# Performance work log

Hardware: AMD Instinct MI355X
Metric: run time of the kernel (lower is better)

Reference implementation:

```python
import jax, jax.numpy as jnp
import numpy as np

NEG_INF = -1e30
NEG_SLOPE = 0.2


def setup_inputs() -> dict:
    key = jax.random.key(0)
    k1, k2, k3, k4, k5 = jax.random.split(key, 5)
    B, N, D, H = 2, 2048, 512, 8
    k = D // H
    return {
        "x": jax.random.normal(k1, (B, N, D), dtype=jnp.float32),
        "A": jax.random.randint(k2, (B, N, N), 0, 2, dtype=jnp.int32),
        "W_proj": jax.random.normal(k3, (D, D), dtype=jnp.float32) * (1.0 / np.sqrt(D)),
        "W_att": jax.random.normal(k4, (H, 2 * k), dtype=jnp.float32) * (1.0 / np.sqrt(2 * k)),
        "b_att": jax.random.normal(k5, (H,), dtype=jnp.float32) * 0.01,
    }


def reference(x, A, W_proj, W_att, b_att):
    # x: [B, N, D_in]; A: [B, N, N]; W_proj: [D_in, D_out]; W_att: [H, 2k]; b_att: [H]
    B, N, _ = x.shape
    H, two_k = W_att.shape
    k = two_k // 2
    xp = jnp.einsum('bnd,do->bno', x, W_proj)            # [B, N, H*k]
    xh = xp.reshape(B, N, H, k).transpose(0, 2, 1, 3)    # [B, H, N, k]
    # Additive attention: score(i,j) = leaky_relu(w[:k]@x_i + w[k:]@x_j + b).
    # Decompose instead of materializing the O(N^2 * 2k) concat tensor.
    a_src = jnp.einsum('bhnk,hk->bhn', xh, W_att[:, :k])  # contribution of node i
    a_dst = jnp.einsum('bhnk,hk->bhn', xh, W_att[:, k:])  # contribution of node j
    scores = a_src[:, :, :, None] + a_dst[:, :, None, :] + b_att[None, :, None, None]
    scores = jax.nn.leaky_relu(scores, negative_slope=NEG_SLOPE)  # [B, H, N, N]
    mask = (A > 0)[:, None, :, :]
    scores = jnp.where(mask, scores, NEG_INF)
    att = jax.nn.softmax(scores, axis=-1)
    out = jax.nn.relu(jnp.einsum('bhij,bhjk->bhik', att, xh))  # [B, H, N, k]
    return out.transpose(0, 2, 1, 3).reshape(B, N, H * k)
```

## Files before the change

kernel.cpp:

```cpp
#include <hip/hip_runtime.h>
#include <cstdint>
#include <cstddef>

#define NEG_SLOPE 0.2f
#define LOG2E 1.4426950408889634f

#define BB 2
#define NN 2048
#define DD 512
#define HH 8
#define KK 64

typedef _Float16 half8 __attribute__((ext_vector_type(8)));
typedef _Float16 half4 __attribute__((ext_vector_type(4)));
typedef _Float16 half2v __attribute__((ext_vector_type(2)));
typedef float floatx4 __attribute__((ext_vector_type(4)));

#define X16T_OFF  ((size_t)0)
#define WT_OFF    ((size_t)4194304)
#define XHT_OFF   ((size_t)4718592)
#define ASRC_OFF  ((size_t)8912896)
#define AFP_OFF   ((size_t)9043968)
#define AFM_OFF   ((size_t)9109504)
#define ADMAX_OFF ((size_t)9175040)
#define MW_OFF    ((size_t)9183232)

#if __has_builtin(__builtin_amdgcn_global_load_lds)
#define GLL(gsrc, lbase, lane) \
    __builtin_amdgcn_global_load_lds((const __attribute__((address_space(1))) void*)(gsrc), \
                                     (__attribute__((address_space(3))) void*)(lbase), 16, 0, 0)
#else
#define GLL(gsrc, lbase, lane) \
    (*(uint4*)((char*)(lbase) + (size_t)(lane) * 16) = *(const uint4*)(gsrc))
#endif

__device__ __forceinline__ unsigned pkmm(unsigned Ep2, unsigned fp,
                                         unsigned Em2, unsigned fm) {
    union U { unsigned u; half2v h; };
    U a, b, c, d, r;
    a.u = Ep2; b.u = fp; c.u = Em2; d.u = fm;
    r.h = __builtin_elementwise_max(a.h * b.h, c.h * d.h);
    return r.u;
}

__global__ __launch_bounds__(256) void k_prep(const float* __restrict__ x,
                                              const float* __restrict__ Wp,
                                              _Float16* __restrict__ x16t,
                                              _Float16* __restrict__ WT) {
    __shared__ float tile[64][65];
    const int tid = threadIdx.x;
    const int bi = blockIdx.x;
    if (bi < 256) {
        const int r = tid & 15, cg = tid >> 4;
        const float* srow = x + (size_t)(bi * 16 + r) * DD;
        _Float16* obase = x16t + ((size_t)bi * 64) * 128 + r * 8;
#pragma unroll
        for (int q = 0; q < 4; ++q) {
            const int chunk = q * 16 + cg;
            float4 v0 = *(const float4*)(srow + chunk * 8);
            float4 v1 = *(const float4*)(srow + chunk * 8 + 4);
            half8 hv;
            hv[0] = (_Float16)v0.x; hv[1] = (_Float16)v0.y;
            hv[2] = (_Float16)v0.z; hv[3] = (_Float16)v0.w;
            hv[4] = (_Float16)v1.x; hv[5] = (_Float16)v1.y;
            hv[6] = (_Float16)v1.z; hv[7] = (_Float16)v1.w;
            *(half8*)(obase + (size_t)chunk * 128) = hv;
        }
    } else {
        const int wb = bi - 256;
        const int d0 = (wb >> 3) * 64, o0 = (wb & 7) * 64;
        const int r = tid >> 2, cq = tid & 3;
#pragma unroll
        for (int qq = 0; qq < 4; ++qq) {
            float4 v = *(const float4*)&Wp[(size_t)(d0 + r) * DD + o0 + cq * 16 + qq * 4];
            tile[r][cq * 16 + qq * 4 + 0] = v.x;
            tile[r][cq * 16 + qq * 4 + 1] = v.y;
            tile[r][cq * 16 + qq * 4 + 2] = v.z;
            tile[r][cq * 16 + qq * 4 + 3] = v.w;
        }
        __syncthreads();
#pragma unroll
        for (int qq = 0; qq < 2; ++qq) {
            half8 hv;
#pragma unroll
            for (int e = 0; e < 8; ++e) hv[e] = (_Float16)tile[cq * 16 + qq * 8 + e][r];
            *(half8*)&WT[(size_t)(o0 + r) * DD + d0 + cq * 16 + qq * 8] = hv;
        }
    }
}

__global__ __launch_bounds__(256) void k_pj(const int* __restrict__ A,
                                            const _Float16* __restrict__ x16t,
                                            const _Float16* __restrict__ WT,
                                            const float* __restrict__ Watt,
                                            unsigned long long* __restrict__ mwT,
                                            _Float16* __restrict__ xhT2,
                                            float* __restrict__ asrc,
                                            unsigned* __restrict__ aFp_g,
                                            unsigned* __restrict__ aFm_g,
                                            float* __restrict__ admax) {
    __shared__ __align__(16) char smem[65536];
    const int tid = threadIdx.x;
    const int bi = blockIdx.x;
    const int r3 = bi % 3;

    if (r3 != 2) {
        unsigned long long (*mwt)[4] = (unsigned long long (*)[4])smem;
        const int mid = (bi / 3) * 2 + r3;
        const int w = tid >> 6, lane = tid & 63;
        const int b = mid >> 9, n0 = (mid & 511) * 4;
        const int* Arow = A + ((size_t)b * NN + n0 + w) * NN + lane;
        int v[32];
#pragma unroll
        for (int c = 0; c < 32; ++c) v[c] = Arow[c * 64];
#pragma unroll
        for (int c = 0; c < 32; ++c) {
            unsigned long long m = __ballot(v[c] != 0);
            if (lane == 0) mwt[c][w] = m;
        }
        __syncthreads();
        if (tid < 128) {
            const int c = tid >> 2, rl = tid & 3;
            mwT[((size_t)b * 32 + c) * NN + n0 + rl] = mwt[c][rl];
        }
        return;
    }

    _Float16* bt = (_Float16*)smem;
    const int pid = bi / 3;
    const int mtile = pid >> 3, h = pid & 7;
    const int m0 = mtile * 64;
    {
        const int cir = tid & 63, wv4 = tid >> 6;
        const char* gsrc = (const char*)(WT + (size_t)h * 64 * DD);
        char* lbase = (char*)bt;
#pragma unroll
        for (int q = 0; q < 16; ++q) {
            const int row = q * 4 + wv4;
            *(uint4*)(lbase + row * 1024 + ((cir ^ (row & 7)) * 16)) =
                *(const uint4*)(gsrc + (size_t)row * 1024 + cir * 16);
        }
    }
    __syncthreads();
    const int w = tid >> 6, l = tid & 63, li = l & 15, p = l >> 4;
    const char* bbase = (const char*)bt;
    const _Float16* abase = x16t + ((size_t)(mtile * 4 + w)) * 64 * 128 + li * 8;
    floatx4 acc[4] = {};
    for (int k0 = 0; k0 < DD; k0 += 32) {
        const int ch = (k0 >> 3) + p;
        half8 a = *(const half8*)(abase + (size_t)ch * 128);
#pragma unroll
        for (int ct = 0; ct < 4; ++ct) {
            const int row = ct * 16 + li;
            half8 bfr = *(const half8*)(bbase + row * 1024 + ((ch ^ (li & 7)) * 16));
            acc[ct] = __builtin_amdgcn_mfma_f32_16x16x32_f16(a, bfr, acc[ct], 0, 0, 0);
        }
    }
    const int b = m0 >> 11, n0m = m0 & (NN - 1);
    const int c = n0m >> 6;
    const int bh = b * HH + h;
    {
        char* tb2 = (char*)xhT2 + ((size_t)(bh * 32 + c)) * 8192;
        const int colchunk = w * 2 + (p >> 1);
        const int sub = (p & 1) * 8;
#pragma unroll
        for (int ct = 0; ct < 4; ++ct) {
            const int kk = ct * 16 + li;
            half4 hv;
#pragma unroll
            for (int r = 0; r < 4; ++r) hv[r] = (_Float16)acc[ct][r];
            *(half4*)(tb2 + kk * 128 + ((colchunk ^ (kk & 7)) << 4) + sub) = hv;
        }
    }
    float w1[4], w2[4];
#pragma unroll
    for (int ct = 0; ct < 4; ++ct) {
        w1[ct] = Watt[h * 128 + ct * 16 + li];
        w2[ct] = Watt[h * 128 + 64 + ct * 16 + li];
    }
    float s1v[4], s2v[4];
    float mx = -1e30f;
#pragma unroll
    for (int r = 0; r < 4; ++r) {
        float s1 = 0.f, s2 = 0.f;
#pragma unroll
        for (int ct = 0; ct < 4; ++ct) { s1 += acc[ct][r] * w1[ct]; s2 += acc[ct][r] * w2[ct]; }
#pragma unroll
        for (int d = 1; d < 16; d <<= 1) { s1 += __shfl_xor(s1, d, 64); s2 += __shfl_xor(s2, d, 64); }
        s1v[r] = s1; s2v[r] = s2;
        mx = fmaxf(mx, s2);
    }
    mx = fmaxf(mx, __shfl_xor(mx, 16, 64));
    mx = fmaxf(mx, __shfl_xor(mx, 32, 64));
    if (l == 0) admax[bh * 128 + (mtile & 31) * 4 + w] = mx;
    if (li == 0) {
        const int nb = n0m + w * 16 + p * 4;
        *(float4*)&asrc[bh * NN + nb] = make_float4(s1v[0], s1v[1], s1v[2], s1v[3]);
        union { half2v h; unsigned u; } q;
        unsigned fpw[2], fmw[2];
#pragma unroll
        for (int pr = 0; pr < 2; ++pr) {
            q.h[0] = (_Float16)exp2f(s2v[2 * pr] * LOG2E);
            q.h[1] = (_Float16)exp2f(s2v[2 * pr + 1] * LOG2E);
            fpw[pr] = q.u;
            q.h[0] = (_Float16)exp2f(NEG_SLOPE * s2v[2 * pr] * LOG2E);
            q.h[1] = (_Float16)exp2f(NEG_SLOPE * s2v[2 * pr + 1] * LOG2E);
            fmw[pr] = q.u;
        }
        const int wb = (bh * NN + nb) >> 1;
        *(uint2*)&aFp_g[wb] = make_uint2(fpw[0], fpw[1]);
        *(uint2*)&aFm_g[wb] = make_uint2(fmw[0], fmw[1]);
    }
}

__global__ __launch_bounds__(256) void k_attn(const _Float16* __restrict__ xhT2,
                                              const float* __restrict__ asrc,
                                              const unsigned* __restrict__ aFp,
                                              const unsigned* __restrict__ aFm,
                                              const float* __restrict__ admax,
                                              const unsigned long long* __restrict__ mwT,
                                              const float* __restrict__ batt,
                                              float* __restrict__ out) {
    __shared__ __align__(16) _Float16 vt[2][2][4096];
    __shared__ __align__(16) unsigned aFpl[2][2][32];
    __shared__ __align__(16) unsigned aFml[2][2][32];
    __shared__ unsigned long long mwl[2][2][32];
    __shared__ float accd_s[2][16];
    __shared__ float amx_s;

    const int tid = threadIdx.x;
    const int w = tid >> 6, l = tid & 63, li = l & 15, p = l >> 4;
    const int g = w & 1, wr = w >> 1;
    const int bid = blockIdx.x;
    const int bh = bid >> 6, it = bid & 63;
    const int b = bh >> 3, h = bh & (HH - 1);
    const int i0 = it * 32;

    const _Float16* vbase = xhT2 + (size_t)bh * 32 * 4096;

    {
#pragma unroll
        for (int q = 0; q < 4; ++q) {
            const int chunk = (wr * 4 + q) * 64 + l;
            GLL(vbase + (size_t)g * 4096 + chunk * 8, &vt[g][0][(wr * 4 + q) * 512], l);
        }
        if (tid < 128) {
            const int arr = tid >> 6, par = (tid >> 5) & 1, wd = tid & 31;
            const unsigned v = (arr ? aFm : aFp)[bh * 1024 + par * 32 + wd];
            if (arr) aFml[par][0][wd] = v; else aFpl[par][0][wd] = v;
        }
        if (tid < 64) mwl[tid >> 5][0][tid & 31] =
            mwT[((size_t)b * 32 + (tid >> 5)) * NN + i0 + (tid & 31)];
    }
    if (w == 0) {
        float mx = fmaxf(admax[bh * 128 + l], admax[bh * 128 + 64 + l]);
#pragma unroll
        for (int d = 1; d < 64; d <<= 1) mx = fmaxf(mx, __shfl_xor(mx, d, 64));
        if (l == 0) amx_s = mx;
    }
    __syncthreads();

    const float am = amx_s;
    const float bbv = batt[h];
    const int i = i0 + wr * 16 + li;
    const float ai = (asrc[bh * NN + i] + bbv) * LOG2E;
    const float tb = ai + am * LOG2E;
    const float Mi = fmaxf(tb, NEG_SLOPE * tb);
    union { half2v h; unsigned u; } epk, emk;
    epk.h[0] = epk.h[1] = (_Float16)exp2f(ai - Mi);
    emk.h[0] = emk.h[1] = (_Float16)exp2f(NEG_SLOPE * ai - Mi);
    const unsigned Ep2 = epk.u, Em2 = emk.u;
    floatx4 acc[4] = {};
    floatx4 accd = {};
    half8 ones;
#pragma unroll
    for (int e = 0; e < 8; ++e) ones[e] = (_Float16)1.0f;

    unsigned raf = 0; unsigned long long rmw = 0;
    for (int ci = 0; ci < 16; ++ci) {
        const int buf = ci & 1;
        char* vtg = (char*)&vt[g][buf][0];
        if (ci < 15) {
            const int cb = 2 * (ci + 1);
            const int cn = cb + g;
#pragma unroll
            for (int q = 0; q < 4; ++q) {
                const int chunk = (wr * 4 + q) * 64 + l;
                GLL(vbase + (size_t)cn * 4096 + chunk * 8, &vt[g][buf ^ 1][(wr * 4 + q) * 512], l);
            }
            if (tid < 128) {
                const int arr = tid >> 6, par = (tid >> 5) & 1, wd = tid & 31;
                raf = (arr ? aFm : aFp)[bh * 1024 + (cb + par) * 32 + wd];
            }
            if (tid < 64) rmw = mwT[((size_t)b * 32 + cb + (tid >> 5)) * NN + i0 + (tid & 31)];
        }
        const unsigned long long mword = mwl[g][buf][wr * 16 + li];
#pragma unroll
        for (int js = 0; js < 2; ++js) {
            const int wb = js * 16 + p * 4;
            const uint4 Fp4 = *(const uint4*)&aFpl[g][buf][wb];
            const uint4 Fm4 = *(const uint4*)&aFml[g][buf][wb];
            const unsigned m8 = (unsigned)(mword >> (js * 32 + p * 8)) & 0xFFu;
            const unsigned fpv[4] = {Fp4.x, Fp4.y, Fp4.z, Fp4.w};
            const unsigned fmv[4] = {Fm4.x, Fm4.y, Fm4.z, Fm4.w};
            union { unsigned u[4]; half8 h; } afu;
#pragma unroll
            for (int pi = 0; pi < 4; ++pi) {
                const unsigned m2 = (m8 >> (2 * pi)) & 3u;
                const unsigned mk = ((m2 & 1u) ? 0x0000FFFFu : 0u) |
                                    ((m2 & 2u) ? 0xFFFF0000u : 0u);
                afu.u[pi] = pkmm(Ep2, fpv[pi], Em2, fmv[pi]) & mk;
            }
            const half8 af = afu.h;
            accd = __builtin_amdgcn_mfma_f32_16x16x32_f16(af, ones, accd, 0, 0, 0);
#pragma unroll
            for (int ct = 0; ct < 4; ++ct) {
                const half8 bf = *(const half8*)(vtg + (ct * 16 + li) * 128 +
                                                 (((js * 4 + p) ^ (li & 7)) << 4));
                acc[ct] = __builtin_amdgcn_mfma_f32_16x16x32_f16(af, bf, acc[ct], 0, 0, 0);
            }
        }
        if (ci < 15) {
            if (tid < 128) {
                const int arr = tid >> 6, par = (tid >> 5) & 1, wd = tid & 31;
                if (arr) aFml[par][buf ^ 1][wd] = raf; else aFpl[par][buf ^ 1][wd] = raf;
            }
            if (tid < 64) mwl[tid >> 5][buf ^ 1][tid & 31] = rmw;
        }
        __syncthreads();
    }

    float* accs = (float*)&vt[0][0][0];
    if (g == 1) {
#pragma unroll
        for (int ct = 0; ct < 4; ++ct)
#pragma unroll
            for (int r = 0; r < 4; ++r)
                accs[(wr * 16 + p * 4 + r) * 64 + ct * 16 + li] = acc[ct][r];
        if (li == 0) {
#pragma unroll
            for (int r = 0; r < 4; ++r) accd_s[wr][p * 4 + r] = accd[r];
        }
    }
    __syncthreads();
    if (g == 0) {
#pragma unroll
        for (int r = 0; r < 4; ++r) {
            const float d = accd[r] + accd_s[wr][p * 4 + r];
            const float inv = 1.f / fmaxf(d, 1e-30f);
            const int irow = i0 + wr * 16 + p * 4 + r;
            float* orow = out + ((size_t)b * NN + irow) * DD + h * KK;
#pragma unroll
            for (int ct = 0; ct < 4; ++ct) {
                const float v = (acc[ct][r] + accs[(wr * 16 + p * 4 + r) * 64 + ct * 16 + li]) * inv;
                orow[ct * 16 + li] = fmaxf(v, 0.f);
            }
        }
    }
}

extern "C" void kernel_launch(void* const* d_in, const int* in_sizes, int n_in,
                              void* d_out, int out_size, void* d_ws, size_t ws_size,
                              hipStream_t stream) {
    const float* x    = (const float*)d_in[0];
    const int*   A    = (const int*)d_in[1];
    const float* Wp   = (const float*)d_in[2];
    const float* Watt = (const float*)d_in[3];
    const float* batt = (const float*)d_in[4];
    float* out = (float*)d_out;

    char* ws = (char*)d_ws;
    _Float16* x16t = (_Float16*)(ws + X16T_OFF);
    _Float16* WT   = (_Float16*)(ws + WT_OFF);
    _Float16* xhT2 = (_Float16*)(ws + XHT_OFF);
    float* asrc  = (float*)(ws + ASRC_OFF);
    unsigned* aFp = (unsigned*)(ws + AFP_OFF);
    unsigned* aFm = (unsigned*)(ws + AFM_OFF);
    float* admax = (float*)(ws + ADMAX_OFF);
    unsigned long long* mwT = (unsigned long long*)(ws + MW_OFF);

    k_prep<<<dim3(320), 256, 0, stream>>>(x, Wp, x16t, WT);
    k_pj<<<dim3(1536), 256, 0, stream>>>(A, x16t, WT, Watt, mwT, xhT2, asrc, aFp, aFm, admax);
    k_attn<<<dim3(BB * HH * 64), 256, 0, stream>>>(xhT2, asrc, aFp, aFm, admax, mwT, batt, out);
}
```

Baseline: 51.67 us.

## Triple-buffer attention V tiles with partial vmcnt barriers for deeper prefetch

```diff
diff --git a/kernel.cpp b/kernel.cpp
--- a/kernel.cpp
+++ b/kernel.cpp
@@ -33,6 +33,9 @@
 #define GLL(gsrc, lbase, lane) \
     (*(uint4*)((char*)(lbase) + (size_t)(lane) * 16) = *(const uint4*)(gsrc))
 #endif
+
+#define ABAR4() asm volatile("s_waitcnt vmcnt(4)\n\ts_waitcnt lgkmcnt(0)\n\ts_barrier" ::: "memory")
+#define ABAR0() asm volatile("s_waitcnt vmcnt(0)\n\ts_waitcnt lgkmcnt(0)\n\ts_barrier" ::: "memory")
 
 __device__ __forceinline__ unsigned pkmm(unsigned Ep2, unsigned fp,
                                          unsigned Em2, unsigned fm) {
@@ -221,10 +224,10 @@
                                               const unsigned long long* __restrict__ mwT,
                                               const float* __restrict__ batt,
                                               float* __restrict__ out) {
-    __shared__ __align__(16) _Float16 vt[2][2][4096];
-    __shared__ __align__(16) unsigned aFpl[2][2][32];
-    __shared__ __align__(16) unsigned aFml[2][2][32];
-    __shared__ unsigned long long mwl[2][2][32];
+    __shared__ __align__(16) _Float16 vt[2][3][4096];
+    __shared__ __align__(16) unsigned aFpl[2][3][32];
+    __shared__ __align__(16) unsigned aFml[2][3][32];
+    __shared__ unsigned long long mwl[2][3][32];
     __shared__ float accd_s[2][16];
     __shared__ float amx_s;
 
@@ -237,20 +240,21 @@
     const int i0 = it * 32;
 
     const _Float16* vbase = xhT2 + (size_t)bh * 32 * 4096;
-
-    {
-#pragma unroll
-        for (int q = 0; q < 4; ++q) {
-            const int chunk = (wr * 4 + q) * 64 + l;
-            GLL(vbase + (size_t)g * 4096 + chunk * 8, &vt[g][0][(wr * 4 + q) * 512], l);
-        }
-        if (tid < 128) {
-            const int arr = tid >> 6, par = (tid >> 5) & 1, wd = tid & 31;
-            const unsigned v = (arr ? aFm : aFp)[bh * 1024 + par * 32 + wd];
-            if (arr) aFml[par][0][wd] = v; else aFpl[par][0][wd] = v;
-        }
-        if (tid < 64) mwl[tid >> 5][0][tid & 31] =
-            mwT[((size_t)b * 32 + (tid >> 5)) * NN + i0 + (tid & 31)];
+    const int sarr = tid >> 6, spar = (tid >> 5) & 1, swd = tid & 31;
+
+#pragma unroll
+    for (int t = 0; t < 2; ++t) {
+        unsigned raf0 = 0; unsigned long long rmw0 = 0;
+        if (tid < 128) raf0 = (sarr ? aFm : aFp)[bh * 1024 + (2 * t + spar) * 32 + swd];
+        if (tid < 64)  rmw0 = mwT[((size_t)b * 32 + 2 * t + (tid >> 5)) * NN + i0 + (tid & 31)];
+        __builtin_amdgcn_sched_barrier(0);
+        const int cn = 2 * t + g;
+#pragma unroll
+        for (int q = 0; q < 4; ++q)
+            GLL(vbase + (size_t)cn * 4096 + ((wr * 4 + q) * 64 + l) * 8,
+                &vt[g][t][(wr * 4 + q) * 512], l);
+        if (tid < 128) { if (sarr) aFml[spar][t][swd] = raf0; else aFpl[spar][t][swd] = raf0; }
+        if (tid < 64)  mwl[tid >> 5][t][tid & 31] = rmw0;
     }
     if (w == 0) {
         float mx = fmaxf(admax[bh * 128 + l], admax[bh * 128 + 64 + l]);
@@ -258,7 +262,7 @@
         for (int d = 1; d < 64; d <<= 1) mx = fmaxf(mx, __shfl_xor(mx, d, 64));
         if (l == 0) amx_s = mx;
     }
-    __syncthreads();
+    ABAR4();
 
     const float am = amx_s;
     const float bbv = batt[h];
@@ -266,9 +270,9 @@
     const float ai = (asrc[bh * NN + i] + bbv) * LOG2E;
     const float tb = ai + am * LOG2E;
     const float Mi = fmaxf(tb, NEG_SLOPE * tb);
-    union { half2v h; unsigned u; } epk, emk;
-    epk.h[0] = epk.h[1] = (_Float16)exp2f(ai - Mi);
-    emk.h[0] = emk.h[1] = (_Float16)exp2f(NEG_SLOPE * ai - Mi);
+    union { half2v hh; unsigned u; } epk, emk;
+    epk.hh[0] = epk.hh[1] = (_Float16)exp2f(ai - Mi);
+    emk.hh[0] = emk.hh[1] = (_Float16)exp2f(NEG_SLOPE * ai - Mi);
     const unsigned Ep2 = epk.u, Em2 = emk.u;
     floatx4 acc[4] = {};
     floatx4 accd = {};
@@ -276,30 +280,28 @@
 #pragma unroll
     for (int e = 0; e < 8; ++e) ones[e] = (_Float16)1.0f;
 
-    unsigned raf = 0; unsigned long long rmw = 0;
     for (int ci = 0; ci < 16; ++ci) {
-        const int buf = ci & 1;
-        char* vtg = (char*)&vt[g][buf][0];
-        if (ci < 15) {
-            const int cb = 2 * (ci + 1);
-            const int cn = cb + g;
-#pragma unroll
-            for (int q = 0; q < 4; ++q) {
-                const int chunk = (wr * 4 + q) * 64 + l;
-                GLL(vbase + (size_t)cn * 4096 + chunk * 8, &vt[g][buf ^ 1][(wr * 4 + q) * 512], l);
-            }
-            if (tid < 128) {
-                const int arr = tid >> 6, par = (tid >> 5) & 1, wd = tid & 31;
-                raf = (arr ? aFm : aFp)[bh * 1024 + (cb + par) * 32 + wd];
-            }
-            if (tid < 64) rmw = mwT[((size_t)b * 32 + cb + (tid >> 5)) * NN + i0 + (tid & 31)];
-        }
-        const unsigned long long mword = mwl[g][buf][wr * 16 + li];
+        const int slot = ci % 3;
+        const char* vtg = (const char*)&vt[g][slot][0];
+        const int tn = ci + 2;
+        unsigned raf = 0; unsigned long long rmw = 0;
+        if (tn < 16) {
+            if (tid < 128) raf = (sarr ? aFm : aFp)[bh * 1024 + (2 * tn + spar) * 32 + swd];
+            if (tid < 64)  rmw = mwT[((size_t)b * 32 + 2 * tn + (tid >> 5)) * NN + i0 + (tid & 31)];
+            __builtin_amdgcn_sched_barrier(0);
+            const int sn = tn % 3;
+            const int cn = 2 * tn + g;
+#pragma unroll
+            for (int q = 0; q < 4; ++q)
+                GLL(vbase + (size_t)cn * 4096 + ((wr * 4 + q) * 64 + l) * 8,
+                    &vt[g][sn][(wr * 4 + q) * 512], l);
+        }
+        const unsigned long long mword = mwl[g][slot][wr * 16 + li];
 #pragma unroll
         for (int js = 0; js < 2; ++js) {
             const int wb = js * 16 + p * 4;
-            const uint4 Fp4 = *(const uint4*)&aFpl[g][buf][wb];
-            const uint4 Fm4 = *(const uint4*)&aFml[g][buf][wb];
+            const uint4 Fp4 = *(const uint4*)&aFpl[g][slot][wb];
+            const uint4 Fm4 = *(const uint4*)&aFml[g][slot][wb];
             const unsigned m8 = (unsigned)(mword >> (js * 32 + p * 8)) & 0xFFu;
             const unsigned fpv[4] = {Fp4.x, Fp4.y, Fp4.z, Fp4.w};
             const unsigned fmv[4] = {Fm4.x, Fm4.y, Fm4.z, Fm4.w};
@@ -320,14 +322,12 @@
                 acc[ct] = __builtin_amdgcn_mfma_f32_16x16x32_f16(af, bf, acc[ct], 0, 0, 0);
             }
         }
-        if (ci < 15) {
-            if (tid < 128) {
-                const int arr = tid >> 6, par = (tid >> 5) & 1, wd = tid & 31;
-                if (arr) aFml[par][buf ^ 1][wd] = raf; else aFpl[par][buf ^ 1][wd] = raf;
-            }
-            if (tid < 64) mwl[tid >> 5][buf ^ 1][tid & 31] = rmw;
-        }
-        __syncthreads();
+        if (tn < 16) {
+            const int sn = tn % 3;
+            if (tid < 128) { if (sarr) aFml[spar][sn][swd] = raf; else aFpl[spar][sn][swd] = raf; }
+            if (tid < 64)  mwl[tid >> 5][sn][tid & 31] = rmw;
+        }
+        if (ci < 13) ABAR4(); else ABAR0();
     }
 
     float* accs = (float*)&vt[0][0][0];
```

Result: slower. 61.55 us (+19.1%).

## Load V tiles directly from global memory and split key chunks across four waves

Applied to the files above, without the earlier changes.

```diff
diff --git a/kernel.cpp b/kernel.cpp
--- a/kernel.cpp
+++ b/kernel.cpp
@@ -24,15 +24,6 @@
 #define AFM_OFF   ((size_t)9109504)
 #define ADMAX_OFF ((size_t)9175040)
 #define MW_OFF    ((size_t)9183232)
-
-#if __has_builtin(__builtin_amdgcn_global_load_lds)
-#define GLL(gsrc, lbase, lane) \
-    __builtin_amdgcn_global_load_lds((const __attribute__((address_space(1))) void*)(gsrc), \
-                                     (__attribute__((address_space(3))) void*)(lbase), 16, 0, 0)
-#else
-#define GLL(gsrc, lbase, lane) \
-    (*(uint4*)((char*)(lbase) + (size_t)(lane) * 16) = *(const uint4*)(gsrc))
-#endif
 
 __device__ __forceinline__ unsigned pkmm(unsigned Ep2, unsigned fp,
                                          unsigned Em2, unsigned fm) {
@@ -161,15 +152,13 @@
     const int bh = b * HH + h;
     {
         char* tb2 = (char*)xhT2 + ((size_t)(bh * 32 + c)) * 8192;
-        const int colchunk = w * 2 + (p >> 1);
-        const int sub = (p & 1) * 8;
 #pragma unroll
         for (int ct = 0; ct < 4; ++ct) {
             const int kk = ct * 16 + li;
             half4 hv;
 #pragma unroll
             for (int r = 0; r < 4; ++r) hv[r] = (_Float16)acc[ct][r];
-            *(half4*)(tb2 + kk * 128 + ((colchunk ^ (kk & 7)) << 4) + sub) = hv;
+            *(half4*)(tb2 + kk * 128 + w * 32 + p * 8) = hv;
         }
     }
     float w1[4], w2[4];
@@ -221,37 +210,18 @@
                                               const unsigned long long* __restrict__ mwT,
                                               const float* __restrict__ batt,
                                               float* __restrict__ out) {
-    __shared__ __align__(16) _Float16 vt[2][2][4096];
-    __shared__ __align__(16) unsigned aFpl[2][2][32];
-    __shared__ __align__(16) unsigned aFml[2][2][32];
-    __shared__ unsigned long long mwl[2][2][32];
-    __shared__ float accd_s[2][16];
+    __shared__ float accs[3][32][64];
+    __shared__ float accd_s[3][32];
     __shared__ float amx_s;
 
     const int tid = threadIdx.x;
     const int w = tid >> 6, l = tid & 63, li = l & 15, p = l >> 4;
-    const int g = w & 1, wr = w >> 1;
-    const int bid = blockIdx.x;
-    const int bh = bid >> 6, it = bid & 63;
+    const int g = w;
+    const int lb = ((blockIdx.x & 7) << 7) | (blockIdx.x >> 3);
+    const int bh = lb >> 6, it = lb & 63;
     const int b = bh >> 3, h = bh & (HH - 1);
     const int i0 = it * 32;
 
-    const _Float16* vbase = xhT2 + (size_t)bh * 32 * 4096;
-
-    {
-#pragma unroll
-        for (int q = 0; q < 4; ++q) {
-            const int chunk = (wr * 4 + q) * 64 + l;
-            GLL(vbase + (size_t)g * 4096 + chunk * 8, &vt[g][0][(wr * 4 + q) * 512], l);
-        }
-        if (tid < 128) {
-            const int arr = tid >> 6, par = (tid >> 5) & 1, wd = tid & 31;
-            const unsigned v = (arr ? aFm : aFp)[bh * 1024 + par * 32 + wd];
-            if (arr) aFml[par][0][wd] = v; else aFpl[par][0][wd] = v;
-        }
-        if (tid < 64) mwl[tid >> 5][0][tid & 31] =
-            mwT[((size_t)b * 32 + (tid >> 5)) * NN + i0 + (tid & 31)];
-    }
     if (w == 0) {
         float mx = fmaxf(admax[bh * 128 + l], admax[bh * 128 + 64 + l]);
 #pragma unroll
@@ -260,100 +230,104 @@
     }
     __syncthreads();
 
-    const float am = amx_s;
+    const float amL = amx_s * LOG2E;
     const float bbv = batt[h];
-    const int i = i0 + wr * 16 + li;
-    const float ai = (asrc[bh * NN + i] + bbv) * LOG2E;
-    const float tb = ai + am * LOG2E;
-    const float Mi = fmaxf(tb, NEG_SLOPE * tb);
-    union { half2v h; unsigned u; } epk, emk;
-    epk.h[0] = epk.h[1] = (_Float16)exp2f(ai - Mi);
-    emk.h[0] = emk.h[1] = (_Float16)exp2f(NEG_SLOPE * ai - Mi);
-    const unsigned Ep2 = epk.u, Em2 = emk.u;
-    floatx4 acc[4] = {};
-    floatx4 accd = {};
+    const float ai0 = (asrc[bh * NN + i0 + li] + bbv) * LOG2E;
+    const float ai1 = (asrc[bh * NN + i0 + 16 + li] + bbv) * LOG2E;
+    const float tb0 = ai0 + amL, tb1 = ai1 + amL;
+    const float Mi0 = fmaxf(tb0, NEG_SLOPE * tb0);
+    const float Mi1 = fmaxf(tb1, NEG_SLOPE * tb1);
+    union { half2v hh; unsigned u; } cv;
+    cv.hh[0] = cv.hh[1] = (_Float16)exp2f(ai0 - Mi0);             const unsigned Ep0 = cv.u;
+    cv.hh[0] = cv.hh[1] = (_Float16)exp2f(NEG_SLOPE * ai0 - Mi0); const unsigned Em0 = cv.u;
+    cv.hh[0] = cv.hh[1] = (_Float16)exp2f(ai1 - Mi1);             const unsigned Ep1 = cv.u;
+    cv.hh[0] = cv.hh[1] = (_Float16)exp2f(NEG_SLOPE * ai1 - Mi1); const unsigned Em1 = cv.u;
+
+    floatx4 acc0[4] = {}, acc1[4] = {};
+    floatx4 accd0 = {}, accd1 = {};
     half8 ones;
 #pragma unroll
     for (int e = 0; e < 8; ++e) ones[e] = (_Float16)1.0f;
 
-    unsigned raf = 0; unsigned long long rmw = 0;
-    for (int ci = 0; ci < 16; ++ci) {
-        const int buf = ci & 1;
-        char* vtg = (char*)&vt[g][buf][0];
-        if (ci < 15) {
-            const int cb = 2 * (ci + 1);
-            const int cn = cb + g;
-#pragma unroll
-            for (int q = 0; q < 4; ++q) {
-                const int chunk = (wr * 4 + q) * 64 + l;
-                GLL(vbase + (size_t)cn * 4096 + chunk * 8, &vt[g][buf ^ 1][(wr * 4 + q) * 512], l);
-            }
-            if (tid < 128) {
-                const int arr = tid >> 6, par = (tid >> 5) & 1, wd = tid & 31;
-                raf = (arr ? aFm : aFp)[bh * 1024 + (cb + par) * 32 + wd];
-            }
-            if (tid < 64) rmw = mwT[((size_t)b * 32 + cb + (tid >> 5)) * NN + i0 + (tid & 31)];
-        }
-        const unsigned long long mword = mwl[g][buf][wr * 16 + li];
+    const char* vtile = (const char*)(xhT2 + (size_t)bh * 32 * 4096);
+    const unsigned long long* mwb = mwT + (size_t)b * 32 * NN + i0;
+    const unsigned* fpb = aFp + bh * 1024;
+    const unsigned* fmb = aFm + bh * 1024;
+
+#pragma unroll 2
+    for (int t = 0; t < 8; ++t) {
+        const int c = t * 4 + g;
+        const unsigned long long mw0 = mwb[(size_t)c * NN + li];
+        const unsigned long long mw1 = mwb[(size_t)c * NN + 16 + li];
+        const char* tb = vtile + (size_t)c * 8192;
 #pragma unroll
         for (int js = 0; js < 2; ++js) {
-            const int wb = js * 16 + p * 4;
-            const uint4 Fp4 = *(const uint4*)&aFpl[g][buf][wb];
-            const uint4 Fm4 = *(const uint4*)&aFml[g][buf][wb];
-            const unsigned m8 = (unsigned)(mword >> (js * 32 + p * 8)) & 0xFFu;
+            const uint4 Fp4 = *(const uint4*)&fpb[c * 32 + js * 16 + p * 4];
+            const uint4 Fm4 = *(const uint4*)&fmb[c * 32 + js * 16 + p * 4];
+            const unsigned m80 = (unsigned)(mw0 >> (js * 32 + p * 8)) & 0xFFu;
+            const unsigned m81 = (unsigned)(mw1 >> (js * 32 + p * 8)) & 0xFFu;
             const unsigned fpv[4] = {Fp4.x, Fp4.y, Fp4.z, Fp4.w};
             const unsigned fmv[4] = {Fm4.x, Fm4.y, Fm4.z, Fm4.w};
-            union { unsigned u[4]; half8 h; } afu;
+            union { unsigned u[4]; half8 h; } af0u, af1u;
 #pragma unroll
             for (int pi = 0; pi < 4; ++pi) {
-                const unsigned m2 = (m8 >> (2 * pi)) & 3u;
-                const unsigned mk = ((m2 & 1u) ? 0x0000FFFFu : 0u) |
-                                    ((m2 & 2u) ? 0xFFFF0000u : 0u);
-                afu.u[pi] = pkmm(Ep2, fpv[pi], Em2, fmv[pi]) & mk;
-            }
-            const half8 af = afu.h;
-            accd = __builtin_amdgcn_mfma_f32_16x16x32_f16(af, ones, accd, 0, 0, 0);
+                const unsigned m2a = (m80 >> (2 * pi)) & 3u;
+                const unsigned mka = ((m2a & 1u) ? 0x0000FFFFu : 0u) |
+                                     ((m2a & 2u) ? 0xFFFF0000u : 0u);
+                af0u.u[pi] = pkmm(Ep0, fpv[pi], Em0, fmv[pi]) & mka;
+                const unsigned m2b = (m81 >> (2 * pi)) & 3u;
+                const unsigned mkb = ((m2b & 1u) ? 0x0000FFFFu : 0u) |
+                                     ((m2b & 2u) ? 0xFFFF0000u : 0u);
+                af1u.u[pi] = pkmm(Ep1, fpv[pi], Em1, fmv[pi]) & mkb;
+            }
+            const half8 af0 = af0u.h, af1 = af1u.h;
+            accd0 = __builtin_amdgcn_mfma_f32_16x16x32_f16(af0, ones, accd0, 0, 0, 0);
+            accd1 = __builtin_amdgcn_mfma_f32_16x16x32_f16(af1, ones, accd1, 0, 0, 0);
 #pragma unroll
             for (int ct = 0; ct < 4; ++ct) {
-                const half8 bf = *(const half8*)(vtg + (ct * 16 + li) * 128 +
-                                                 (((js * 4 + p) ^ (li & 7)) << 4));
-                acc[ct] = __builtin_amdgcn_mfma_f32_16x16x32_f16(af, bf, acc[ct], 0, 0, 0);
-            }
-        }
-        if (ci < 15) {
-            if (tid < 128) {
-                const int arr = tid >> 6, par = (tid >> 5) & 1, wd = tid & 31;
-                if (arr) aFml[par][buf ^ 1][wd] = raf; else aFpl[par][buf ^ 1][wd] = raf;
-            }
-            if (tid < 64) mwl[tid >> 5][buf ^ 1][tid & 31] = rmw;
-        }
-        __syncthreads();
-    }
-
-    float* accs = (float*)&vt[0][0][0];
-    if (g == 1) {
+                const half8 bf = *(const half8*)(tb + (ct * 16 + li) * 128 + js * 64 + p * 16);
+                acc0[ct] = __builtin_amdgcn_mfma_f32_16x16x32_f16(af0, bf, acc0[ct], 0, 0, 0);
+                acc1[ct] = __builtin_amdgcn_mfma_f32_16x16x32_f16(af1, bf, acc1[ct], 0, 0, 0);
+            }
+        }
+    }
+
+    if (g != 0) {
+        const int s = g - 1;
 #pragma unroll
         for (int ct = 0; ct < 4; ++ct)
 #pragma unroll
-            for (int r = 0; r < 4; ++r)
-                accs[(wr * 16 + p * 4 + r) * 64 + ct * 16 + li] = acc[ct][r];
+            for (int r = 0; r < 4; ++r) {
+                accs[s][p * 4 + r][ct * 16 + li] = acc0[ct][r];
+                accs[s][16 + p * 4 + r][ct * 16 + li] = acc1[ct][r];
+            }
         if (li == 0) {
 #pragma unroll
-            for (int r = 0; r < 4; ++r) accd_s[wr][p * 4 + r] = accd[r];
+            for (int r = 0; r < 4; ++r) {
+                accd_s[s][p * 4 + r] = accd0[r];
+                accd_s[s][16 + p * 4 + r] = accd1[r];
+            }
         }
     }
     __syncthreads();
     if (g == 0) {
 #pragma unroll
-        for (int r = 0; r < 4; ++r) {
-            const float d = accd[r] + accd_s[wr][p * 4 + r];
-            const float inv = 1.f / fmaxf(d, 1e-30f);
-            const int irow = i0 + wr * 16 + p * 4 + r;
-            float* orow = out + ((size_t)b * NN + irow) * DD + h * KK;
-#pragma unroll
-            for (int ct = 0; ct < 4; ++ct) {
-                const float v = (acc[ct][r] + accs[(wr * 16 + p * 4 + r) * 64 + ct * 16 + li]) * inv;
-                orow[ct * 16 + li] = fmaxf(v, 0.f);
+        for (int f = 0; f < 2; ++f) {
+#pragma unroll
+            for (int r = 0; r < 4; ++r) {
+                const int row = f * 16 + p * 4 + r;
+                float d = (f ? accd1[r] : accd0[r]) +
+                          accd_s[0][row] + accd_s[1][row] + accd_s[2][row];
+                const float inv = 1.f / fmaxf(d, 1e-30f);
+                float* orow = out + ((size_t)b * NN + i0 + row) * DD + h * KK;
+                const floatx4* accf = f ? acc1 : acc0;
+#pragma unroll
+                for (int ct = 0; ct < 4; ++ct) {
+                    const int col = ct * 16 + li;
+                    const float v = (accf[ct][r] + accs[0][row][col] +
+                                     accs[1][row][col] + accs[2][row][col]) * inv;
+                    orow[col] = fmaxf(v, 0.f);
+                }
             }
         }
     }
```

After: 78.71 us. 1.52x slower.
